# Performance work log

Measured on AMD Instinct MI355X. Metric: run time of the kernel, lower is better.

## Reference

```python
import jax, jax.numpy as jnp
import numpy as np

B, S, NF, SD, D, FF, H, L = 32, 512, 124, 204, 512, 2048, 8, 4
DH = D // H
POSE_D = (D // H) * 1  # nheads_pose = 1
MAX_LEN = 5000


def make_pe(max_len, d):
    # sinusoidal positional encoding buffer, shape [max_len, 1, d]
    pos = jnp.arange(max_len, dtype=jnp.float32)[:, None]
    div = jnp.exp(jnp.arange(0, d, 2, dtype=jnp.float32) * (-np.log(10000.0) / d))
    pe = jnp.zeros((max_len, d), jnp.float32)
    pe = pe.at[:, 0::2].set(jnp.sin(pos * div)).at[:, 1::2].set(jnp.cos(pos * div))
    return pe[:, None, :]


def layer_norm(x, g, b, eps=1e-5):
    m = jnp.mean(x, -1, keepdims=True)
    v = jnp.mean((x - m) ** 2, -1, keepdims=True)
    return (x - m) / jnp.sqrt(v + eps) * g + b


def leaky_relu(x):
    return jnp.where(x >= 0, x, 0.2 * x)


def setup_inputs() -> dict:
    key = jax.random.key(0)
    ks = iter(jax.random.split(key, 48))

    def nrm(shape, s=0.02):
        return jax.random.normal(next(ks), shape, jnp.float32) * s

    return dict(
        x=jax.random.normal(next(ks), (B, S, NF), jnp.float32),
        timesteps=jax.random.randint(next(ks), (B,), 0, 1000),
        sparse_emb=jax.random.normal(next(ks), (B, S, SD), jnp.float32),
        W_lmk=nrm((SD, D)), b_lmk=jnp.zeros((D,)), g_lmk=jnp.ones((D,)), be_lmk=jnp.zeros((D,)),
        W_in=nrm((NF, D)), b_in=jnp.zeros((D,)), g_in=jnp.ones((D,)), be_in=jnp.zeros((D,)),
        W_merge=nrm((2 * D, D)), b_merge=jnp.zeros((D,)),
        Wt1=nrm((D, D)), bt1=jnp.zeros((D,)), Wt2=nrm((D, D)), bt2=jnp.zeros((D,)),
        in_proj_w=nrm((L, D, 3 * D)), in_proj_b=jnp.zeros((L, 3 * D)),
        out_proj_w=nrm((L, D, D)), out_proj_b=jnp.zeros((L, D)),
        ln1_g=jnp.ones((L, D)), ln1_b=jnp.zeros((L, D)),
        ln2_g=jnp.ones((L, D)), ln2_b=jnp.zeros((L, D)),
        W_ff1=nrm((L, D, FF)), b_ff1=jnp.zeros((L, FF)),
        W_ff2=nrm((L, FF, D)), b_ff2=jnp.zeros((L, D)),
        W_pose=nrm((POSE_D, 24)), b_pose=jnp.zeros((24,)),
        W_expr=nrm((D - POSE_D, 100)), b_expr=jnp.zeros((100,)),
    )


def reference(x, timesteps, sparse_emb,
              W_lmk, b_lmk, g_lmk, be_lmk,
              W_in, b_in, g_in, be_in,
              W_merge, b_merge,
              Wt1, bt1, Wt2, bt2,
              in_proj_w, in_proj_b, out_proj_w, out_proj_b,
              ln1_g, ln1_b, ln2_g, ln2_b,
              W_ff1, b_ff1, W_ff2, b_ff2,
              W_pose, b_pose, W_expr, b_expr):
    pe = make_pe(MAX_LEN, D)                      # [max_len, 1, D]
    # TimestepEmbedder: pe[timesteps] -> [B,1,D] -> MLP -> permute -> [1,B,D]
    ts = pe[timesteps]
    ts = jax.nn.silu(ts @ Wt1 + bt1) @ Wt2 + bt2
    ts_emb = jnp.transpose(ts, (1, 0, 2))
    # Lmk3dProcess / InputProcess: permute to seq-first, Linear+LN+LeakyReLU(0.2)
    lmk = leaky_relu(layer_norm(jnp.transpose(sparse_emb, (1, 0, 2)) @ W_lmk + b_lmk, g_lmk, be_lmk))
    xi = leaky_relu(layer_norm(jnp.transpose(x, (1, 0, 2)) @ W_in + b_in, g_in, be_in))
    h = jnp.concatenate([lmk, xi], -1) @ W_merge + b_merge   # [S,B,D]
    h = jnp.concatenate([ts_emb, h], 0)                      # [S+1,B,D]
    h = h + pe[:S + 1]                                       # pos enc (dropout off in eval)
    scale = 1.0 / np.sqrt(DH)
    T = S + 1
    for l in range(L):  # post-norm nn.TransformerEncoderLayer, gelu
        qkv = h @ in_proj_w[l] + in_proj_b[l]
        q, k, v = jnp.split(qkv, 3, -1)
        q = q.reshape(T, B, H, DH)
        k = k.reshape(T, B, H, DH)
        v = v.reshape(T, B, H, DH)
        att = jax.nn.softmax(jnp.einsum('tbhd,sbhd->bhts', q, k) * scale, axis=-1)
        o = jnp.einsum('bhts,sbhd->tbhd', att, v).reshape(T, B, D)
        h = layer_norm(h + o @ out_proj_w[l] + out_proj_b[l], ln1_g[l], ln1_b[l])
        f = jax.nn.gelu(h @ W_ff1[l] + b_ff1[l], approximate=False) @ W_ff2[l] + b_ff2[l]
        h = layer_norm(h + f, ln2_g[l], ln2_b[l])
    enc = h[1:]  # drop timestep token, [S,B,D]
    pose = jnp.transpose(enc[:, :, :POSE_D] @ W_pose + b_pose, (1, 0, 2))   # [B,S,24]
    expr = jnp.transpose(enc[:, :, POSE_D:] @ W_expr + b_expr, (1, 0, 2))   # [B,S,100]
    return jnp.concatenate([pose, expr], -1)                                # [B,S,124]
```

## Files before the change

kernel.cpp:

```cpp
#include <hip/hip_runtime.h>
#include <cmath>

#define B_ 32
#define S_ 512
#define NF_ 124
#define SD_ 204
#define D_ 512
#define FF_ 2048
#define H_ 8
#define L_ 4
#define T_ 513
#define TB_ 16416
#define SB_ 16384
#define PE_ROWS 1024

typedef unsigned short u16;
typedef __attribute__((ext_vector_type(8))) short bf16x8;
typedef __attribute__((ext_vector_type(4))) float f32x4;

__device__ __forceinline__ u16 f2bf(float f) {
  unsigned int u = __float_as_uint(f);
  unsigned int r = u + 0x7fff + ((u >> 16) & 1);
  return (u16)(r >> 16);
}
__device__ __forceinline__ float bf2f(u16 x) {
  return __uint_as_float((unsigned int)x << 16);
}

__global__ void pe_kernel(float* __restrict__ pe) {
  int p = blockIdx.x;
  int i = threadIdx.x;
  float div = expf(-(float)(2 * i) * (9.210340371976184f / 512.0f));
  float ang = (float)p * div;
  pe[p * 512 + 2 * i]     = sinf(ang);
  pe[p * 512 + 2 * i + 1] = cosf(ang);
}

__global__ void transpose_sb_bf(const float* __restrict__ in, u16* __restrict__ out,
                                int C, int Cpad, int total) {
  int idx = blockIdx.x * 256 + threadIdx.x;
  if (idx >= total) return;
  int c  = idx % Cpad;
  int sb = idx / Cpad;
  int b  = sb & (B_ - 1);
  int s  = sb >> 5;
  out[idx] = (c < C) ? f2bf(in[((size_t)b * S_ + s) * C + c]) : (u16)0;
}

__global__ __launch_bounds__(256) void wtrans_kernel(const float* __restrict__ W,
                                                     u16* __restrict__ Wt,
                                                     int K, int N,
                                                     long in_stride, long out_stride) {
  __shared__ float t[32][33];
  int l = blockIdx.z;
  W  += (size_t)l * in_stride;
  Wt += (size_t)l * out_stride;
  int n0 = blockIdx.x * 32, k0 = blockIdx.y * 32;
  int r = threadIdx.x >> 3;
  int c4 = (threadIdx.x & 7) * 4;
  float4 v = *(const float4*)(W + (size_t)(k0 + r) * N + n0 + c4);
  t[r][c4 + 0] = v.x; t[r][c4 + 1] = v.y; t[r][c4 + 2] = v.z; t[r][c4 + 3] = v.w;
  __syncthreads();
  u16* dst = Wt + (size_t)(n0 + r) * K + k0 + c4;
  for (int i = 0; i < 4; i++) dst[i] = f2bf(t[c4 + i][r]);
}

__global__ __launch_bounds__(256) void wtrans_pad_kernel(const float* __restrict__ W,
                                                         u16* __restrict__ Wt,
                                                         int K, int Kpad, int N) {
  __shared__ float t[32][33];
  int n0 = blockIdx.x * 32, k0 = blockIdx.y * 32;
  int r = threadIdx.x >> 3;
  int c4 = (threadIdx.x & 7) * 4;
  float4 v = make_float4(0.f, 0.f, 0.f, 0.f);
  if (k0 + r < K) v = *(const float4*)(W + (size_t)(k0 + r) * N + n0 + c4);
  t[r][c4 + 0] = v.x; t[r][c4 + 1] = v.y; t[r][c4 + 2] = v.z; t[r][c4 + 3] = v.w;
  __syncthreads();
  u16* dst = Wt + (size_t)(n0 + r) * Kpad + k0 + c4;
  for (int i = 0; i < 4; i++) dst[i] = f2bf(t[c4 + i][r]);
}

__global__ void head_prep_kernel(const float* __restrict__ Wp, const float* __restrict__ bp,
                                 const float* __restrict__ We, const float* __restrict__ be,
                                 u16* __restrict__ head_t, float* __restrict__ head_b) {
  int idx = blockIdx.x * 256 + threadIdx.x;
  int n = idx >> 9, k = idx & 511;
  float v = 0.f;
  if (n < 24) { if (k < 64) v = Wp[k * 24 + n]; }
  else if (n < 124) { if (k >= 64) v = We[(size_t)(k - 64) * 100 + (n - 24)]; }
  head_t[idx] = f2bf(v);
  if (idx < 128) head_b[idx] = (idx < 24) ? bp[idx] : ((idx < 124) ? be[idx - 24] : 0.f);
}

__global__ void ts_gather_kernel(const int* __restrict__ tsteps,
                                 const float* __restrict__ pe,
                                 u16* __restrict__ A) {
  int idx = blockIdx.x * 256 + threadIdx.x;
  int b = idx >> 9, k = idx & 511;
  A[idx] = f2bf(pe[(size_t)tsteps[b] * 512 + k]);
}

template<int BM, int BN, int WM, int WN>
__global__ __launch_bounds__(512) void gemm_bf16_t(
    const u16* __restrict__ A, const u16* __restrict__ Bt,
    const float* __restrict__ bias,
    u16* __restrict__ Cb, float* __restrict__ Cf,
    int M, int N, int K, int flags)
{
  constexpr int MT = WM / 16, NT = WN / 16;
  constexpr int ACH = BM * 8;
  constexpr int TCH = (BM + BN) * 8;
  constexpr int NC  = TCH / 512;
  constexpr int WROWS = BM / WM;
  __shared__ u16 sm[(BM + BN) * 64];
  int tid = threadIdx.x;
  int m0 = blockIdx.y * BM, n0 = blockIdx.x * BN;
  int wave = tid >> 6, lane = tid & 63;
  int wm = (wave % WROWS) * WM, wn = (wave / WROWS) * WN;
  int lm = lane & 15, kq = lane >> 4;

  f32x4 acc[MT][NT];
#pragma unroll
  for (int i = 0; i < MT; i++)
#pragma unroll
    for (int j = 0; j < NT; j++) acc[i][j] = (f32x4){0.f, 0.f, 0.f, 0.f};

  const u16* gp[NC];
  u16* lp[NC];
#pragma unroll
  for (int i = 0; i < NC; i++) {
    int c = tid + i * 512;
    if (c < ACH) {
      int p = c / (BM * 4), cp = c % (BM * 4);
      int r = cp >> 2, kk = p * 32 + (cp & 3) * 8;
      int row = m0 + r; if (row > M - 1) row = M - 1;
      gp[i] = A + (size_t)row * K + kk;
    } else {
      int cb = c - ACH;
      int p = cb / (BN * 4), cp = cb % (BN * 4);
      int r = cp >> 2, kk = p * 32 + (cp & 3) * 8;
      int row = n0 + r; if (row > N - 1) row = N - 1;
      gp[i] = Bt + (size_t)row * K + kk;
    }
    lp[i] = sm + (size_t)c * 8;
  }

  for (int k0 = 0; k0 < K; k0 += 64) {
#pragma unroll
    for (int i = 0; i < NC; i++)
      __builtin_amdgcn_global_load_lds(
          (const __attribute__((address_space(1))) void*)(gp[i] + k0),
          (__attribute__((address_space(3))) void*)lp[i], 16, 0, 0);
    __syncthreads();
#pragma unroll
    for (int st = 0; st < 2; st++) {
      bf16x8 af[MT], bg[NT];
#pragma unroll
      for (int i = 0; i < MT; i++)
        af[i] = *(const bf16x8*)&sm[st * BM * 32 + (wm + i * 16 + lm) * 32 + kq * 8];
#pragma unroll
      for (int j = 0; j < NT; j++)
        bg[j] = *(const bf16x8*)&sm[BM * 64 + st * BN * 32 + (wn + j * 16 + lm) * 32 + kq * 8];
#pragma unroll
      for (int i = 0; i < MT; i++)
#pragma unroll
        for (int j = 0; j < NT; j++)
          acc[i][j] = __builtin_amdgcn_mfma_f32_16x16x32_bf16(af[i], bg[j], acc[i][j], 0, 0, 0);
    }
    __syncthreads();
  }

  if (flags & 4) {
#pragma unroll
    for (int j = 0; j < NT; j++) {
      int gn = n0 + wn + j * 16 + lm;
      float bv = bias[gn];
#pragma unroll
      for (int i = 0; i < MT; i++) {
        int gm = m0 + wm + i * 16 + kq * 4;
#pragma unroll
        for (int r = 0; r < 4; r++) {
          if (gm + r < M && gn < 124) {
            int bb = (gm + r) & (B_ - 1), ss = (gm + r) >> 5;
            Cf[((size_t)bb * S_ + ss) * 124 + gn] = acc[i][j][r] + bv;
          }
        }
      }
    }
    return;
  }

#pragma unroll
  for (int j = 0; j < NT; j++) {
    int cn = wn + j * 16 + lm;
    float bv = bias[n0 + cn];
#pragma unroll
    for (int i = 0; i < MT; i++) {
      int rm = wm + i * 16 + kq * 4;
#pragma unroll
      for (int r = 0; r < 4; r++) {
        float v = acc[i][j][r] + bv;
        if (flags & 1) v = 0.5f * v * (1.0f + erff(v * 0.70710678118654752f));
        if (flags & 2) v = v / (1.0f + expf(-v));
        sm[(rm + r) * BN + cn] = f2bf(v);
      }
    }
  }
  __syncthreads();
  constexpr int SP = BM * BN / 4096;
#pragma unroll
  for (int pass = 0; pass < SP; pass++) {
    int e = pass * 4096 + tid * 8;
    int r = e / BN, cc = e % BN;
    int gm = m0 + r;
    if (gm < M)
      *(bf16x8*)(Cb + (size_t)gm * N + n0 + cc) = *(const bf16x8*)&sm[r * BN + cc];
  }
}

__device__ __forceinline__ float wave_sum(float v) {
#pragma unroll
  for (int off = 1; off < 64; off <<= 1) v += __shfl_xor(v, off, 64);
  return v;
}

__global__ __launch_bounds__(256) void ln_leaky_concat_kernel(
    const u16* __restrict__ lmk, const u16* __restrict__ xi,
    const float* __restrict__ gl, const float* __restrict__ bl,
    const float* __restrict__ gx, const float* __restrict__ bx,
    u16* __restrict__ cat)
{
  int wave = threadIdx.x >> 6, lane = threadIdx.x & 63;
  int g = blockIdx.x * 4 + wave;
  int r = g >> 1, part = g & 1;
  const u16* src = (part ? xi : lmk) + (size_t)r * 512 + lane * 8;
  const float* gg = (part ? gx : gl) + lane * 8;
  const float* bb = (part ? bx : bl) + lane * 8;
  bf16x8 hv = *(const bf16x8*)src;
  float v[8];
#pragma unroll
  for (int i = 0; i < 8; i++) v[i] = bf2f(((const u16*)&hv)[i]);
  float s = 0.f;
#pragma unroll
  for (int i = 0; i < 8; i++) s += v[i];
  float mean = wave_sum(s) * (1.0f / 512.0f);
  float s2 = 0.f;
#pragma unroll
  for (int i = 0; i < 8; i++) { v[i] -= mean; s2 += v[i] * v[i]; }
  float rs = rsqrtf(wave_sum(s2) * (1.0f / 512.0f) + 1e-5f);
  u16 ov[8];
#pragma unroll
  for (int i = 0; i < 8; i++) {
    float y = v[i] * rs * gg[i] + bb[i];
    y = (y >= 0.f) ? y : 0.2f * y;
    ov[i] = f2bf(y);
  }
  *(bf16x8*)(cat + (size_t)r * 1024 + part * 512 + lane * 8) = *(const bf16x8*)ov;
}

__global__ __launch_bounds__(256) void add_ln_kernel(
    u16* __restrict__ h_bf, const u16* __restrict__ src,
    const float* __restrict__ g, const float* __restrict__ be)
{
  int wave = threadIdx.x >> 6, lane = threadIdx.x & 63;
  int r = blockIdx.x * 4 + wave;
  size_t base = (size_t)r * 512 + lane * 8;
  bf16x8 hv = *(const bf16x8*)&h_bf[base];
  bf16x8 sv = *(const bf16x8*)&src[base];
  float v[8];
#pragma unroll
  for (int i = 0; i < 8; i++)
    v[i] = bf2f(((const u16*)&hv)[i]) + bf2f(((const u16*)&sv)[i]);
  float s = 0.f;
#pragma unroll
  for (int i = 0; i < 8; i++) s += v[i];
  float mean = wave_sum(s) * (1.0f / 512.0f);
  float s2 = 0.f;
#pragma unroll
  for (int i = 0; i < 8; i++) { v[i] -= mean; s2 += v[i] * v[i]; }
  float rs = rsqrtf(wave_sum(s2) * (1.0f / 512.0f) + 1e-5f);
  const float* gg = g + lane * 8;
  const float* bb = be + lane * 8;
  u16 ov[8];
#pragma unroll
  for (int i = 0; i < 8; i++) ov[i] = f2bf(v[i] * rs * gg[i] + bb[i]);
  *(bf16x8*)&h_bf[base] = *(const bf16x8*)ov;
}

__global__ void add_pe_kernel(u16* __restrict__ h_bf, const float* __restrict__ pe) {
  int idx = blockIdx.x * 256 + threadIdx.x;
  int e = idx * 8;
  int j = e & 511;
  int t = (e >> 9) / B_;
  bf16x8 hv = *(const bf16x8*)&h_bf[e];
  const float* pv = &pe[(size_t)t * 512 + j];
  u16 ov[8];
#pragma unroll
  for (int i = 0; i < 8; i++) ov[i] = f2bf(bf2f(((const u16*)&hv)[i]) + pv[i]);
  *(bf16x8*)&h_bf[e] = *(const bf16x8*)ov;
}

__global__ __launch_bounds__(256) void attn_kernel(const u16* __restrict__ qkv,
                                                   u16* __restrict__ o)
{
  __shared__ u16 Ks[64 * 72];
  __shared__ u16 Vt[64 * 72];
  __shared__ u16 Ps[64 * 72];

  int qp = blockIdx.x;
  int bh = blockIdx.y;
  int b  = bh >> 3;
  int hh = bh & 7;
  int tid  = threadIdx.x;
  int wave = tid >> 6, lane = tid & 63;
  int lm = lane & 15, quad = lane >> 4;
  int wm = wave * 16;
  int t0 = qp * 128;
  int nq = (t0 + 64 < T_) ? 2 : 1;

  bf16x8 qf[2][2];
#pragma unroll
  for (int q = 0; q < 2; q++) {
    int t = t0 + q * 64 + wm + lm; if (t > T_ - 1) t = T_ - 1;
    const u16* qp_ = qkv + ((size_t)(t * B_ + b)) * 1536 + hh * 64;
    qf[q][0] = *(const bf16x8*)(qp_ + quad * 8);
    qf[q][1] = *(const bf16x8*)(qp_ + 32 + quad * 8);
  }

  f32x4 o_acc[2][4];
  float lsum[2][4];
#pragma unroll
  for (int q = 0; q < 2; q++)
#pragma unroll
    for (int dt = 0; dt < 4; dt++) {
      o_acc[q][dt] = (f32x4){0.f, 0.f, 0.f, 0.f};
      lsum[q][0] = lsum[q][1] = lsum[q][2] = lsum[q][3] = 0.f;
    }

  const float cs = 0.125f * 1.4426950408889634f;

  for (int s0 = 0; s0 < T_; s0 += 64) {
    __syncthreads();
#pragma unroll
    for (int cc = 0; cc < 2; cc++) {
      int c = tid + cc * 256;
      int sr = c >> 3, db = (c & 7) * 8;
      int s = s0 + sr; if (s > T_ - 1) s = T_ - 1;
      *(bf16x8*)&Ks[sr * 72 + db] =
          *(const bf16x8*)(qkv + ((size_t)(s * B_ + b)) * 1536 + 512 + hh * 64 + db);
    }
#pragma unroll
    for (int cc = 0; cc < 2; cc++) {
      int c = tid + cc * 256;
      int sr = c & 63, db = (c >> 6) * 8;
      int s = s0 + sr; if (s > T_ - 1) s = T_ - 1;
      bf16x8 vv = *(const bf16x8*)(qkv + ((size_t)(s * B_ + b)) * 1536 + 1024 + hh * 64 + db);
      const u16* pv = (const u16*)&vv;
#pragma unroll
      for (int i = 0; i < 8; i++) Vt[(db + i) * 72 + sr] = pv[i];
    }
    __syncthreads();

#pragma unroll
    for (int q = 0; q < 2; q++) {
      if (q >= nq) continue;
      f32x4 sacc[4];
#pragma unroll
      for (int st = 0; st < 4; st++) {
        sacc[st] = (f32x4){0.f, 0.f, 0.f, 0.f};
        bf16x8 k0 = *(const bf16x8*)&Ks[(st * 16 + lm) * 72 + quad * 8];
        bf16x8 k1 = *(const bf16x8*)&Ks[(st * 16 + lm) * 72 + 32 + quad * 8];
        sacc[st] = __builtin_amdgcn_mfma_f32_16x16x32_bf16(qf[q][0], k0, sacc[st], 0, 0, 0);
        sacc[st] = __builtin_amdgcn_mfma_f32_16x16x32_bf16(qf[q][1], k1, sacc[st], 0, 0, 0);
      }
#pragma unroll
      for (int st = 0; st < 4; st++) {
        bool bad = (s0 + st * 16 + lm) >= T_;
#pragma unroll
        for (int r = 0; r < 4; r++) {
          float v = bad ? -10000.f : sacc[st][r] * cs;
          float p = exp2f(v);
          sacc[st][r] = p;
          lsum[q][r] += p;
        }
      }
#pragma unroll
      for (int st = 0; st < 4; st++)
#pragma unroll
        for (int r = 0; r < 4; r++)
          Ps[(wm + quad * 4 + r) * 72 + st * 16 + lm] = f2bf(sacc[st][r]);
#pragma unroll
      for (int ks = 0; ks < 2; ks++) {
        bf16x8 pf = *(const bf16x8*)&Ps[(wm + lm) * 72 + ks * 32 + quad * 8];
#pragma unroll
        for (int dt = 0; dt < 4; dt++) {
          bf16x8 vf = *(const bf16x8*)&Vt[(dt * 16 + lm) * 72 + ks * 32 + quad * 8];
          o_acc[q][dt] = __builtin_amdgcn_mfma_f32_16x16x32_bf16(pf, vf, o_acc[q][dt], 0, 0, 0);
        }
      }
    }
  }

#pragma unroll
  for (int q = 0; q < 2; q++) {
    if (q >= nq) continue;
    float inv[4];
#pragma unroll
    for (int r = 0; r < 4; r++) {
      float s = lsum[q][r];
#pragma unroll
      for (int off = 1; off < 16; off <<= 1) s += __shfl_xor(s, off, 64);
      inv[r] = 1.0f / s;
    }
    __syncthreads();
#pragma unroll
    for (int dt = 0; dt < 4; dt++)
#pragma unroll
      for (int r = 0; r < 4; r++)
        Ps[(wm + quad * 4 + r) * 72 + dt * 16 + lm] = f2bf(o_acc[q][dt][r] * inv[r]);
    int rr = wm + (lane >> 2);
    int db = (lane & 3) * 16;
    int t = t0 + q * 64 + rr;
    if (t < T_) {
      bf16x8 a = *(const bf16x8*)&Ps[rr * 72 + db];
      bf16x8 b8 = *(const bf16x8*)&Ps[rr * 72 + db + 8];
      u16* op = o + ((size_t)(t * B_ + b)) * 512 + hh * 64 + db;
      *(bf16x8*)op = a;
      *(bf16x8*)(op + 8) = b8;
    }
  }
}

extern "C" void kernel_launch(void* const* d_in, const int* in_sizes, int n_in,
                              void* d_out, int out_size, void* d_ws, size_t ws_size,
                              hipStream_t stream) {
  const float* x       = (const float*)d_in[0];
  const int*   tsteps  = (const int*)  d_in[1];
  const float* se      = (const float*)d_in[2];
  const float* W_lmk   = (const float*)d_in[3];
  const float* b_lmk   = (const float*)d_in[4];
  const float* g_lmk   = (const float*)d_in[5];
  const float* be_lmk  = (const float*)d_in[6];
  const float* W_in    = (const float*)d_in[7];
  const float* b_in    = (const float*)d_in[8];
  const float* g_in    = (const float*)d_in[9];
  const float* be_in   = (const float*)d_in[10];
  const float* W_merge = (const float*)d_in[11];
  const float* b_merge = (const float*)d_in[12];
  const float* Wt1     = (const float*)d_in[13];
  const float* bt1     = (const float*)d_in[14];
  const float* Wt2     = (const float*)d_in[15];
  const float* bt2     = (const float*)d_in[16];
  const float* in_proj_w  = (const float*)d_in[17];
  const float* in_proj_b  = (const float*)d_in[18];
  const float* out_proj_w = (const float*)d_in[19];
  const float* out_proj_b = (const float*)d_in[20];
  const float* ln1_g   = (const float*)d_in[21];
  const float* ln1_b   = (const float*)d_in[22];
  const float* ln2_g   = (const float*)d_in[23];
  const float* ln2_b   = (const float*)d_in[24];
  const float* W_ff1   = (const float*)d_in[25];
  const float* b_ff1   = (const float*)d_in[26];
  const float* W_ff2   = (const float*)d_in[27];
  const float* b_ff2   = (const float*)d_in[28];
  const float* W_pose  = (const float*)d_in[29];
  const float* b_pose  = (const float*)d_in[30];
  const float* W_expr  = (const float*)d_in[31];
  const float* b_expr  = (const float*)d_in[32];
  float* out = (float*)d_out;

  float* pe      = (float*)d_ws;
  u16*   h_bf    = (u16*)(pe + (size_t)PE_ROWS * 512);
  u16*   big_bf  = h_bf + (size_t)TB_ * 512;
  u16*   bufO_bf = big_bf + (size_t)TB_ * 2048;
  u16*   bufP_bf = bufO_bf + (size_t)TB_ * 512;
  u16* merge_t = bufP_bf + (size_t)TB_ * 512;
  u16* ip_t    = merge_t + (size_t)512 * 1024;
  u16* op_t    = ip_t    + (size_t)L_ * 1536 * 512;
  u16* ff1_t   = op_t    + (size_t)L_ * 512 * 512;
  u16* ff2_t   = ff1_t   + (size_t)L_ * 2048 * 512;
  u16* lmk_t   = ff2_t   + (size_t)L_ * 512 * 2048;
  u16* xin_t   = lmk_t   + (size_t)512 * 256;
  u16* head_t  = xin_t   + (size_t)512 * 128;
  u16* wt1_t   = head_t  + (size_t)128 * 512;
  u16* wt2_t   = wt1_t   + (size_t)512 * 512;
  u16* ts_in   = wt2_t   + (size_t)512 * 512;
  u16* ts_mid  = ts_in   + (size_t)32 * 512;
  float* head_b = (float*)(ts_mid + (size_t)32 * 512);
  u16* seT_bf = bufO_bf;
  u16* xT_bf  = bufP_bf;
  u16* lmk_bf = big_bf;
  u16* xi_bf  = big_bf + (size_t)SB_ * 512;
  u16* cat_bf = big_bf + (size_t)SB_ * 1024;

  auto g128 = [&](const u16* A, const u16* Bt, const float* bias, u16* Cb,
                  int M, int N, int K, int flags) {
    dim3 grid(N / 128, (M + 127) / 128);
    gemm_bf16_t<128, 128, 32, 64><<<grid, 512, 0, stream>>>(A, Bt, bias, Cb, nullptr, M, N, K, flags);
  };
  auto g64 = [&](const u16* A, const u16* Bt, const float* bias, u16* Cb, float* Cf,
                 int M, int N, int K, int flags) {
    dim3 grid(N / 128, (M + 63) / 64);
    gemm_bf16_t<64, 128, 32, 32><<<grid, 512, 0, stream>>>(A, Bt, bias, Cb, Cf, M, N, K, flags);
  };

  wtrans_kernel<<<dim3(512 / 32, 1024 / 32, 1), 256, 0, stream>>>(
      W_merge, merge_t, 1024, 512, 0, 0);
  wtrans_kernel<<<dim3(1536 / 32, 512 / 32, L_), 256, 0, stream>>>(
      in_proj_w, ip_t, 512, 1536, (long)512 * 1536, (long)1536 * 512);
  wtrans_kernel<<<dim3(512 / 32, 512 / 32, L_), 256, 0, stream>>>(
      out_proj_w, op_t, 512, 512, (long)512 * 512, (long)512 * 512);
  wtrans_kernel<<<dim3(2048 / 32, 512 / 32, L_), 256, 0, stream>>>(
      W_ff1, ff1_t, 512, 2048, (long)512 * 2048, (long)2048 * 512);
  wtrans_kernel<<<dim3(512 / 32, 2048 / 32, L_), 256, 0, stream>>>(
      W_ff2, ff2_t, 2048, 512, (long)2048 * 512, (long)512 * 2048);
  wtrans_kernel<<<dim3(512 / 32, 512 / 32, 1), 256, 0, stream>>>(Wt1, wt1_t, 512, 512, 0, 0);
  wtrans_kernel<<<dim3(512 / 32, 512 / 32, 1), 256, 0, stream>>>(Wt2, wt2_t, 512, 512, 0, 0);
  wtrans_pad_kernel<<<dim3(512 / 32, 256 / 32), 256, 0, stream>>>(W_lmk, lmk_t, SD_, 256, 512);
  wtrans_pad_kernel<<<dim3(512 / 32, 128 / 32), 256, 0, stream>>>(W_in, xin_t, NF_, 128, 512);
  head_prep_kernel<<<(128 * 512) / 256, 256, 0, stream>>>(W_pose, b_pose, W_expr, b_expr,
                                                          head_t, head_b);

  pe_kernel<<<PE_ROWS, 256, 0, stream>>>(pe);
  transpose_sb_bf<<<(SB_ * 256 + 255) / 256, 256, 0, stream>>>(se, seT_bf, SD_, 256, SB_ * 256);
  transpose_sb_bf<<<(SB_ * 128 + 255) / 256, 256, 0, stream>>>(x, xT_bf, NF_, 128, SB_ * 128);
  g64(seT_bf, lmk_t, b_lmk, lmk_bf, nullptr, SB_, 512, 256, 0);
  g64(xT_bf, xin_t, b_in, xi_bf, nullptr, SB_, 512, 128, 0);
  ln_leaky_concat_kernel<<<SB_ * 2 / 4, 256, 0, stream>>>(lmk_bf, xi_bf, g_lmk, be_lmk,
                                                          g_in, be_in, cat_bf);
  g64(cat_bf, merge_t, b_merge, h_bf + (size_t)B_ * 512, nullptr, SB_, 512, 1024, 0);
  ts_gather_kernel<<<(32 * 512) / 256, 256, 0, stream>>>(tsteps, pe, ts_in);
  g64(ts_in, wt1_t, bt1, ts_mid, nullptr, 32, 512, 512, 2);
  g64(ts_mid, wt2_t, bt2, h_bf, nullptr, 32, 512, 512, 0);
  add_pe_kernel<<<TB_ * 512 / 8 / 256, 256, 0, stream>>>(h_bf, pe);

  for (int l = 0; l < L_; l++) {
    g128(h_bf, ip_t + (size_t)l * 1536 * 512, in_proj_b + l * 1536,
         big_bf, TB_, 1536, 512, 0);
    attn_kernel<<<dim3(5, B_ * H_), 256, 0, stream>>>(big_bf, bufO_bf);
    g64(bufO_bf, op_t + (size_t)l * 512 * 512, out_proj_b + l * 512,
        bufP_bf, nullptr, TB_, 512, 512, 0);
    add_ln_kernel<<<TB_ / 4, 256, 0, stream>>>(h_bf, bufP_bf, ln1_g + l * 512, ln1_b + l * 512);
    g128(h_bf, ff1_t + (size_t)l * 2048 * 512, b_ff1 + l * 2048,
         big_bf, TB_, 2048, 512, 1);
    g64(big_bf, ff2_t + (size_t)l * 512 * 2048, b_ff2 + l * 512,
        bufP_bf, nullptr, TB_, 512, 2048, 0);
    add_ln_kernel<<<TB_ / 4, 256, 0, stream>>>(h_bf, bufP_bf, ln2_g + l * 512, ln2_b + l * 512);
  }

  g64(h_bf + (size_t)B_ * 512, head_t, head_b, nullptr, out, SB_, 128, 512, 4);
}
```

Before: 1.421 ms.

## Use 8 waves per attention block, one 16-row query tile each

The attention kernel goes from 256 to 512 threads. Each of the 8 waves now owns its own 16-row query tile instead of 4 waves each looping over two 64-row query halves. K/V staging is spread over twice as many threads, and the P scratch buffer doubles to 128 rows. The aim is more waves in flight per block to hide the MFMA and LDS latency, and fewer registers per thread. The cost is more LDS per block and a possible occupancy limit from 512-thread blocks.

New measurement: 1.419 ms. About the same (-0.1%).

```diff
diff --git a/kernel.cpp b/kernel.cpp
--- a/kernel.cpp
+++ b/kernel.cpp
@@ -300,12 +300,12 @@
   *(bf16x8*)&h_bf[e] = *(const bf16x8*)ov;
 }
 
-__global__ __launch_bounds__(256) void attn_kernel(const u16* __restrict__ qkv,
+__global__ __launch_bounds__(512) void attn_kernel(const u16* __restrict__ qkv,
                                                    u16* __restrict__ o)
 {
   __shared__ u16 Ks[64 * 72];
   __shared__ u16 Vt[64 * 72];
-  __shared__ u16 Ps[64 * 72];
+  __shared__ u16 Ps[128 * 72];
 
   int qp = blockIdx.x;
   int bh = blockIdx.y;
@@ -316,43 +316,32 @@
   int lm = lane & 15, quad = lane >> 4;
   int wm = wave * 16;
   int t0 = qp * 128;
-  int nq = (t0 + 64 < T_) ? 2 : 1;
-
-  bf16x8 qf[2][2];
-#pragma unroll
-  for (int q = 0; q < 2; q++) {
-    int t = t0 + q * 64 + wm + lm; if (t > T_ - 1) t = T_ - 1;
+
+  bf16x8 qf0, qf1;
+  {
+    int t = t0 + wm + lm; if (t > T_ - 1) t = T_ - 1;
     const u16* qp_ = qkv + ((size_t)(t * B_ + b)) * 1536 + hh * 64;
-    qf[q][0] = *(const bf16x8*)(qp_ + quad * 8);
-    qf[q][1] = *(const bf16x8*)(qp_ + 32 + quad * 8);
-  }
-
-  f32x4 o_acc[2][4];
-  float lsum[2][4];
-#pragma unroll
-  for (int q = 0; q < 2; q++)
-#pragma unroll
-    for (int dt = 0; dt < 4; dt++) {
-      o_acc[q][dt] = (f32x4){0.f, 0.f, 0.f, 0.f};
-      lsum[q][0] = lsum[q][1] = lsum[q][2] = lsum[q][3] = 0.f;
-    }
+    qf0 = *(const bf16x8*)(qp_ + quad * 8);
+    qf1 = *(const bf16x8*)(qp_ + 32 + quad * 8);
+  }
+
+  f32x4 o_acc[4];
+  float lsum[4] = {0.f, 0.f, 0.f, 0.f};
+#pragma unroll
+  for (int dt = 0; dt < 4; dt++) o_acc[dt] = (f32x4){0.f, 0.f, 0.f, 0.f};
 
   const float cs = 0.125f * 1.4426950408889634f;
 
   for (int s0 = 0; s0 < T_; s0 += 64) {
     __syncthreads();
-#pragma unroll
-    for (int cc = 0; cc < 2; cc++) {
-      int c = tid + cc * 256;
-      int sr = c >> 3, db = (c & 7) * 8;
+    {
+      int sr = tid >> 3, db = (tid & 7) * 8;
       int s = s0 + sr; if (s > T_ - 1) s = T_ - 1;
       *(bf16x8*)&Ks[sr * 72 + db] =
           *(const bf16x8*)(qkv + ((size_t)(s * B_ + b)) * 1536 + 512 + hh * 64 + db);
     }
-#pragma unroll
-    for (int cc = 0; cc < 2; cc++) {
-      int c = tid + cc * 256;
-      int sr = c & 63, db = (c >> 6) * 8;
+    {
+      int sr = tid & 63, db = (tid >> 6) * 8;
       int s = s0 + sr; if (s > T_ - 1) s = T_ - 1;
       bf16x8 vv = *(const bf16x8*)(qkv + ((size_t)(s * B_ + b)) * 1536 + 1024 + hh * 64 + db);
       const u16* pv = (const u16*)&vv;
@@ -361,66 +350,59 @@
     }
     __syncthreads();
 
-#pragma unroll
-    for (int q = 0; q < 2; q++) {
-      if (q >= nq) continue;
-      f32x4 sacc[4];
-#pragma unroll
-      for (int st = 0; st < 4; st++) {
-        sacc[st] = (f32x4){0.f, 0.f, 0.f, 0.f};
-        bf16x8 k0 = *(const bf16x8*)&Ks[(st * 16 + lm) * 72 + quad * 8];
-        bf16x8 k1 = *(const bf16x8*)&Ks[(st * 16 + lm) * 72 + 32 + quad * 8];
-        sacc[st] = __builtin_amdgcn_mfma_f32_16x16x32_bf16(qf[q][0], k0, sacc[st], 0, 0, 0);
-        sacc[st] = __builtin_amdgcn_mfma_f32_16x16x32_bf16(qf[q][1], k1, sacc[st], 0, 0, 0);
+    f32x4 sacc[4];
+#pragma unroll
+    for (int st = 0; st < 4; st++) {
+      sacc[st] = (f32x4){0.f, 0.f, 0.f, 0.f};
+      bf16x8 k0 = *(const bf16x8*)&Ks[(st * 16 + lm) * 72 + quad * 8];
+      bf16x8 k1 = *(const bf16x8*)&Ks[(st * 16 + lm) * 72 + 32 + quad * 8];
+      sacc[st] = __builtin_amdgcn_mfma_f32_16x16x32_bf16(qf0, k0, sacc[st], 0, 0, 0);
+      sacc[st] = __builtin_amdgcn_mfma_f32_16x16x32_bf16(qf1, k1, sacc[st], 0, 0, 0);
+    }
+#pragma unroll
+    for (int st = 0; st < 4; st++) {
+      bool bad = (s0 + st * 16 + lm) >= T_;
+#pragma unroll
+      for (int r = 0; r < 4; r++) {
+        float v = bad ? -10000.f : sacc[st][r] * cs;
+        float p = exp2f(v);
+        sacc[st][r] = p;
+        lsum[r] += p;
       }
-#pragma unroll
-      for (int st = 0; st < 4; st++) {
-        bool bad = (s0 + st * 16 + lm) >= T_;
-#pragma unroll
-        for (int r = 0; r < 4; r++) {
-          float v = bad ? -10000.f : sacc[st][r] * cs;
-          float p = exp2f(v);
-          sacc[st][r] = p;
-          lsum[q][r] += p;
-        }
+    }
+#pragma unroll
+    for (int st = 0; st < 4; st++)
+#pragma unroll
+      for (int r = 0; r < 4; r++)
+        Ps[(wm + quad * 4 + r) * 72 + st * 16 + lm] = f2bf(sacc[st][r]);
+#pragma unroll
+    for (int ks = 0; ks < 2; ks++) {
+      bf16x8 pf = *(const bf16x8*)&Ps[(wm + lm) * 72 + ks * 32 + quad * 8];
+#pragma unroll
+      for (int dt = 0; dt < 4; dt++) {
+        bf16x8 vf = *(const bf16x8*)&Vt[(dt * 16 + lm) * 72 + ks * 32 + quad * 8];
+        o_acc[dt] = __builtin_amdgcn_mfma_f32_16x16x32_bf16(pf, vf, o_acc[dt], 0, 0, 0);
       }
-#pragma unroll
-      for (int st = 0; st < 4; st++)
-#pragma unroll
-        for (int r = 0; r < 4; r++)
-          Ps[(wm + quad * 4 + r) * 72 + st * 16 + lm] = f2bf(sacc[st][r]);
-#pragma unroll
-      for (int ks = 0; ks < 2; ks++) {
-        bf16x8 pf = *(const bf16x8*)&Ps[(wm + lm) * 72 + ks * 32 + quad * 8];
-#pragma unroll
-        for (int dt = 0; dt < 4; dt++) {
-          bf16x8 vf = *(const bf16x8*)&Vt[(dt * 16 + lm) * 72 + ks * 32 + quad * 8];
-          o_acc[q][dt] = __builtin_amdgcn_mfma_f32_16x16x32_bf16(pf, vf, o_acc[q][dt], 0, 0, 0);
-        }
-      }
-    }
-  }
-
-#pragma unroll
-  for (int q = 0; q < 2; q++) {
-    if (q >= nq) continue;
-    float inv[4];
-#pragma unroll
-    for (int r = 0; r < 4; r++) {
-      float s = lsum[q][r];
-#pragma unroll
-      for (int off = 1; off < 16; off <<= 1) s += __shfl_xor(s, off, 64);
-      inv[r] = 1.0f / s;
-    }
-    __syncthreads();
-#pragma unroll
-    for (int dt = 0; dt < 4; dt++)
-#pragma unroll
-      for (int r = 0; r < 4; r++)
-        Ps[(wm + quad * 4 + r) * 72 + dt * 16 + lm] = f2bf(o_acc[q][dt][r] * inv[r]);
+    }
+  }
+
+  float inv[4];
+#pragma unroll
+  for (int r = 0; r < 4; r++) {
+    float s = lsum[r];
+#pragma unroll
+    for (int off = 1; off < 16; off <<= 1) s += __shfl_xor(s, off, 64);
+    inv[r] = 1.0f / s;
+  }
+#pragma unroll
+  for (int dt = 0; dt < 4; dt++)
+#pragma unroll
+    for (int r = 0; r < 4; r++)
+      Ps[(wm + quad * 4 + r) * 72 + dt * 16 + lm] = f2bf(o_acc[dt][r] * inv[r]);
+  {
     int rr = wm + (lane >> 2);
     int db = (lane & 3) * 16;
-    int t = t0 + q * 64 + rr;
+    int t = t0 + rr;
     if (t < T_) {
       bf16x8 a = *(const bf16x8*)&Ps[rr * 72 + db];
       bf16x8 b8 = *(const bf16x8*)&Ps[rr * 72 + db + 8];
@@ -537,7 +519,7 @@
   for (int l = 0; l < L_; l++) {
     g128(h_bf, ip_t + (size_t)l * 1536 * 512, in_proj_b + l * 1536,
          big_bf, TB_, 1536, 512, 0);
-    attn_kernel<<<dim3(5, B_ * H_), 256, 0, stream>>>(big_bf, bufO_bf);
+    attn_kernel<<<dim3(5, B_ * H_), 512, 0, stream>>>(big_bf, bufO_bf);
     g64(bufO_bf, op_t + (size_t)l * 512 * 512, out_proj_b + l * 512,
         bufP_bf, nullptr, TB_, 512, 512, 0);
     add_ln_kernel<<<TB_ / 4, 256, 0, stream>>>(h_bf, bufP_bf, ln1_g + l * 512, ln1_b + l * 512);
```
